# Performance work log

Hardware: AMD Instinct MI355X
Metric: run time of the kernel (lower is better)

The kernel has to match this reference:

```python
import jax, jax.numpy as jnp
import numpy as np

N, E, G, DIN, DH = 50000, 800000, 256, 128, 128
BN_EPS = 1e-5


def _gin_layer(h, src, dst, W1, b1, gamma, beta, W2, b2):
    # GINConv (eps=0): agg_i = sum_{(j->i) in edges} h_j ; z = agg + h
    agg = jnp.zeros_like(h).at[dst].add(h[src])
    z = agg + h
    z = z @ W1 + b1
    # BatchNorm1d (training mode: batch stats over nodes, biased var)
    mean = z.mean(axis=0)
    var = z.var(axis=0)
    z = gamma * (z - mean) * jax.lax.rsqrt(var + BN_EPS) + beta
    z = jax.nn.relu(z)
    z = z @ W2 + b2
    return jax.nn.relu(z)


def setup_inputs() -> dict:
    key = jax.random.key(0)
    ks = jax.random.split(key, 12)
    x = jax.random.normal(ks[0], (N, DIN), dtype=jnp.float32)
    edge_index = jax.random.randint(ks[1], (2, E), 0, N, dtype=jnp.int32)
    batch = jnp.sort(jax.random.randint(ks[2], (N,), 0, G, dtype=jnp.int32))
    s = 0.05
    W1 = jax.random.normal(ks[3], (7, DIN, DH), dtype=jnp.float32) * s
    b1 = jnp.zeros((7, DH), dtype=jnp.float32)
    gamma = jnp.ones((7, DH), dtype=jnp.float32)
    beta = jnp.zeros((7, DH), dtype=jnp.float32)
    W2 = jax.random.normal(ks[4], (7, DH, DH), dtype=jnp.float32) * s
    b2 = jnp.zeros((7, DH), dtype=jnp.float32)
    Wl1 = jax.random.normal(ks[5], (14 * DH, 14 * DH), dtype=jnp.float32) * s
    bl1 = jnp.zeros((14 * DH,), dtype=jnp.float32)
    Wl2 = jax.random.normal(ks[6], (14 * DH, 1), dtype=jnp.float32) * s
    bl2 = jnp.zeros((1,), dtype=jnp.float32)
    return {"x": x, "edge_index": edge_index, "batch": batch,
            "W1": W1, "b1": b1, "gamma": gamma, "beta": beta,
            "W2": W2, "b2": b2, "Wl1": Wl1, "bl1": bl1,
            "Wl2": Wl2, "bl2": bl2}


def reference(x, edge_index, batch, W1, b1, gamma, beta, W2, b2, Wl1, bl1, Wl2, bl2):
    src, dst = edge_index[0], edge_index[1]
    hs = []
    h = x
    for i in range(7):
        h = _gin_layer(h, src, dst, W1[i], b1[i], gamma[i], beta[i], W2[i], b2[i])
        hs.append(h)
    adds = [jax.ops.segment_sum(hi, batch, num_segments=G) for hi in hs]
    maxs = [jax.ops.segment_max(hi, batch, num_segments=G) for hi in hs]
    h = jnp.concatenate(adds + maxs, axis=1)  # [G, 14*DH]
    h = jax.nn.relu(h @ Wl1 + bl1)
    h = h @ Wl2 + bl2
    return (jax.nn.sigmoid(h), h)
```

## Files before the change

### kernel.cpp

```cpp
#include <hip/hip_runtime.h>
#include <cstdint>
#include <cstddef>

#define NN 50000
#define NE 800000
#define NG 256
#define NLAY 7
#define NBLK1 1563
#define NBUCK 16
#define CAP 18432

typedef float f32x4 __attribute__((ext_vector_type(4)));
typedef __bf16 bf16x8 __attribute__((ext_vector_type(8)));
typedef _Float16 h16x8 __attribute__((ext_vector_type(8)));

__device__ __forceinline__ float4 ld4(const float* p) { return *(const float4*)p; }
__device__ __forceinline__ void addh8(float4& x, float4& y, h16x8 v) {
  x.x += (float)v[0]; x.y += (float)v[1]; x.z += (float)v[2]; x.w += (float)v[3];
  y.x += (float)v[4]; y.y += (float)v[5]; y.z += (float)v[6]; y.w += (float)v[7];
}

__global__ void k_init(const float* __restrict__ x, const float* __restrict__ W1,
                       const float* __restrict__ W2, int* __restrict__ counts,
                       int* __restrict__ gcur, float* __restrict__ pooled,
                       _Float16* __restrict__ hb,
                       __bf16* __restrict__ w1f, __bf16* __restrict__ w2f,
                       float* __restrict__ psums) {
  int i = blockIdx.x * 256 + threadIdx.x;
  if (i < NN) counts[i] = 0;
  if (i < 49) gcur[i] = i * CAP;
  if (i < NLAY * NBUCK * 256) psums[i] = 0.f;
  if (i < NG * 1792) pooled[i] = 0.f;
  if (i < NN * 128) hb[i] = (_Float16)x[i];
  if (i < NLAY * 32768) {
    int l = i >> 15, pos = i & 32767;
    int j = pos & 7, ln = (pos >> 3) & 63, slot = (pos >> 9) & 15, kc = pos >> 13;
    int hl = slot & 1, ctp = (slot >> 1) & 3, hfp = slot >> 3;
    int n = hfp * 64 + ctp * 16 + (ln & 15);
    int k = kc * 32 + ((ln >> 4) << 3) + j;
    float a = W1[l * 16384 + k * 128 + n];
    float b = W2[l * 16384 + k * 128 + n];
    __bf16 ah = (__bf16)a, bh = (__bf16)b;
    w1f[i] = hl ? (__bf16)(a - (float)ah) : ah;
    w2f[i] = hl ? (__bf16)(b - (float)bh) : bh;
  }
}

__global__ void k_hist(const int* __restrict__ edge, int* __restrict__ counts) {
  int e = blockIdx.x * 256 + threadIdx.x;
  if (e < NE) atomicAdd(&counts[edge[NE + e]], 1);
}

__global__ void k_part(const int* __restrict__ counts, int* __restrict__ bsum) {
  __shared__ int sm[256];
  int b = blockIdx.x, t = threadIdx.x;
  int i = b * 256 + t;
  sm[t] = (i < NN) ? counts[i] : 0;
  __syncthreads();
  for (int s = 128; s > 0; s >>= 1) {
    if (t < s) sm[t] += sm[t + s];
    __syncthreads();
  }
  if (t == 0) bsum[b] = sm[0];
}

__global__ void k_bscan(const int* __restrict__ bsum, int* __restrict__ boff,
                        int* __restrict__ row_ptr) {
  __shared__ int sm[256];
  int t = threadIdx.x;
  int v = (t < 196) ? bsum[t] : 0;
  sm[t] = v;
  __syncthreads();
  int val = v;
  for (int off = 1; off < 256; off <<= 1) {
    int o = (t >= off) ? sm[t - off] : 0;
    __syncthreads();
    val += o;
    sm[t] = val;
    __syncthreads();
  }
  if (t < 196) boff[t] = val - v;
  if (t == 255) row_ptr[NN] = val;
}

__global__ void k_rowptr(const int* __restrict__ counts, const int* __restrict__ boff,
                         int* __restrict__ row_ptr) {
  __shared__ int sm[256];
  int b = blockIdx.x, t = threadIdx.x;
  int i = b * 256 + t;
  int c = (i < NN) ? counts[i] : 0;
  sm[t] = c;
  __syncthreads();
  int val = c;
  for (int off = 1; off < 256; off <<= 1) {
    int o = (t >= off) ? sm[t - off] : 0;
    __syncthreads();
    val += o;
    sm[t] = val;
    __syncthreads();
  }
  if (i < NN) row_ptr[i] = val - c + boff[b];
}

__global__ __launch_bounds__(256) void k_binA(const int* __restrict__ edge,
                                              int* __restrict__ gcur,
                                              unsigned int* __restrict__ bins) {
  __shared__ int lh[49], lbase[49], lt[49];
  const int tid = threadIdx.x;
  const int e0 = blockIdx.x * 3125, e1 = e0 + 3125;
  if (tid < 49) { lh[tid] = 0; lt[tid] = 0; }
  __syncthreads();
  for (int e = e0 + tid; e < e1; e += 256)
    atomicAdd(&lh[edge[NE + e] >> 10], 1);
  __syncthreads();
  if (tid < 49) lbase[tid] = atomicAdd(&gcur[tid], lh[tid]);
  __syncthreads();
  for (int e = e0 + tid; e < e1; e += 256) {
    int dst = edge[NE + e], src = edge[e];
    int r = dst >> 10;
    int t = atomicAdd(&lt[r], 1);
    bins[lbase[r] + t] = ((unsigned)dst << 16) | (unsigned)src;
  }
}

__global__ __launch_bounds__(512) void k_binB(const int* __restrict__ row_ptr,
                                              const int* __restrict__ gcur,
                                              const unsigned int* __restrict__ bins,
                                              unsigned short* __restrict__ csr16) {
  __shared__ int lcur[1024];
  __shared__ unsigned short lcsr[24576];
  const int blk = blockIdx.x, tid = threadIdx.x;
  const int base = blk << 10;
  const int nn = (base + 1024 <= NN) ? 1024 : (NN - base);
  const int seg0 = row_ptr[base];
  const int seg1 = row_ptr[(base + 1024 <= NN) ? (base + 1024) : NN];
  for (int i = tid; i < nn; i += 512) lcur[i] = row_ptr[base + i] - seg0;
  __syncthreads();
  const int tot = gcur[blk] - blk * CAP;
  for (int t = tid; t < tot; t += 512) {
    unsigned int p = bins[blk * CAP + t];
    int dst = (int)(p >> 16), src = (int)(p & 0xffffu);
    int pos = atomicAdd(&lcur[dst - base], 1);
    lcsr[pos] = (unsigned short)src;
  }
  __syncthreads();
  for (int i = tid; i < seg1 - seg0; i += 512) csr16[seg0 + i] = lcsr[i];
}

__device__ __forceinline__ void split8(const float4 v0, const float4 v1,
                                       bf16x8& hi, bf16x8& lo) {
  float f[8] = {v0.x, v0.y, v0.z, v0.w, v1.x, v1.y, v1.z, v1.w};
  #pragma unroll
  for (int j = 0; j < 8; ++j) {
    __bf16 h = (__bf16)f[j];
    hi[j] = h;
    lo[j] = (__bf16)(f[j] - (float)h);
  }
}

__device__ __forceinline__ void mfma_phase32(
    int tid, const __bf16* __restrict__ wf, float (*zs)[132], f32x4 acc[2])
{
  const int wv = tid >> 6;
  const int stripe = wv >> 2, half = (wv >> 1) & 1, cpair = wv & 1;
  const int lane = tid & 63, q = lane >> 4, m = lane & 15;
  #pragma unroll
  for (int kc = 0; kc < 4; ++kc) {
    const int k0 = kc * 32 + q * 8;
    float4 v0 = *(const float4*)&zs[stripe * 16 + m][k0];
    float4 v1 = *(const float4*)&zs[stripe * 16 + m][k0 + 4];
    bf16x8 ah, al;
    split8(v0, v1, ah, al);
    #pragma unroll
    for (int j = 0; j < 2; ++j) {
      const int ct = cpair * 2 + j;
      const int sbase = (half * 4 + ct) * 2;
      const __bf16* bp = wf + (((size_t)(kc * 16 + sbase) * 64 + lane) << 3);
      bf16x8 bh = *(const bf16x8*)bp;
      bf16x8 bl = *(const bf16x8*)(bp + 512);
      acc[j] = __builtin_amdgcn_mfma_f32_16x16x32_bf16(ah, bh, acc[j], 0, 0, 0);
      acc[j] = __builtin_amdgcn_mfma_f32_16x16x32_bf16(ah, bl, acc[j], 0, 0, 0);
      acc[j] = __builtin_amdgcn_mfma_f32_16x16x32_bf16(al, bh, acc[j], 0, 0, 0);
    }
  }
  __syncthreads();
}

__global__ __launch_bounds__(512, 8) void k_fused1(
    const _Float16* __restrict__ hb, const int* __restrict__ row_ptr,
    const unsigned short* __restrict__ csr_src, const __bf16* __restrict__ wf,
    const float* __restrict__ bias, _Float16* __restrict__ zb,
    float* __restrict__ ps)
{
  __shared__ float zs[32][132];
  const int tid = threadIdx.x;
  const int m0 = blockIdx.x * 32;

  {
    const int lr = tid >> 4;
    const int sub = tid & 15;
    const int r = m0 + lr;
    const int c0 = sub << 3;
    float4 a0 = make_float4(0.f, 0.f, 0.f, 0.f), a1 = a0;
    if (r < NN) {
      addh8(a0, a1, *(const h16x8*)(hb + ((size_t)r << 7) + c0));
      int e = row_ptr[r], e1 = row_ptr[r + 1];
      for (; e + 7 < e1; e += 8) {
        const h16x8 v0 = *(const h16x8*)(hb + ((size_t)csr_src[e + 0] << 7) + c0);
        const h16x8 v1 = *(const h16x8*)(hb + ((size_t)csr_src[e + 1] << 7) + c0);
        const h16x8 v2 = *(const h16x8*)(hb + ((size_t)csr_src[e + 2] << 7) + c0);
        const h16x8 v3 = *(const h16x8*)(hb + ((size_t)csr_src[e + 3] << 7) + c0);
        const h16x8 v4 = *(const h16x8*)(hb + ((size_t)csr_src[e + 4] << 7) + c0);
        const h16x8 v5 = *(const h16x8*)(hb + ((size_t)csr_src[e + 5] << 7) + c0);
        const h16x8 v6 = *(const h16x8*)(hb + ((size_t)csr_src[e + 6] << 7) + c0);
        const h16x8 v7 = *(const h16x8*)(hb + ((size_t)csr_src[e + 7] << 7) + c0);
        h16x8 t0 = v0 + v1, t1 = v2 + v3, t2 = v4 + v5, t3 = v6 + v7;
        h16x8 u0 = t0 + t1, u1 = t2 + t3;
        addh8(a0, a1, u0 + u1);
      }
      if (e + 3 < e1) {
        const h16x8 v0 = *(const h16x8*)(hb + ((size_t)csr_src[e + 0] << 7) + c0);
        const h16x8 v1 = *(const h16x8*)(hb + ((size_t)csr_src[e + 1] << 7) + c0);
        const h16x8 v2 = *(const h16x8*)(hb + ((size_t)csr_src[e + 2] << 7) + c0);
        const h16x8 v3 = *(const h16x8*)(hb + ((size_t)csr_src[e + 3] << 7) + c0);
        h16x8 t0 = v0 + v1, t1 = v2 + v3;
        addh8(a0, a1, t0 + t1);
        e += 4;
      }
      if (e + 1 < e1) {
        const h16x8 v0 = *(const h16x8*)(hb + ((size_t)csr_src[e + 0] << 7) + c0);
        const h16x8 v1 = *(const h16x8*)(hb + ((size_t)csr_src[e + 1] << 7) + c0);
        addh8(a0, a1, v0 + v1);
        e += 2;
      }
      if (e < e1)
        addh8(a0, a1, *(const h16x8*)(hb + ((size_t)csr_src[e] << 7) + c0));
    }
    *(float4*)&zs[lr][c0 + 0] = a0;
    *(float4*)&zs[lr][c0 + 4] = a1;
  }
  __syncthreads();

  const int wv = tid >> 6;
  const int stripe = wv >> 2, half = (wv >> 1) & 1, cpair = wv & 1;
  const int lane = tid & 63, q = lane >> 4, m = lane & 15;
  f32x4 acc[2] = {};
  mfma_phase32(tid, wf, zs, acc);

  float* red_s = (float*)zs;
  float* red_q = red_s + 1152;
  const int sl = stripe * 4 + q;
  #pragma unroll
  for (int j = 0; j < 2; ++j) {
    const int ct = cpair * 2 + j;
    const int col = half * 64 + ct * 16 + m;
    const float bb = bias[col];
    float s = 0.f, qq = 0.f;
    #pragma unroll
    for (int i = 0; i < 4; ++i) {
      int r = m0 + stripe * 16 + q * 4 + i;
      if (r < NN) {
        float o = acc[j][i] + bb;
        zb[((size_t)r << 7) + col] = (_Float16)o;
        s += o; qq += o * o;
      }
    }
    red_s[col * 9 + sl] = s;
    red_q[col * 9 + sl] = qq;
  }
  __syncthreads();
  if (tid < 128) {
    float s = 0.f, qq = 0.f;
    #pragma unroll
    for (int k = 0; k < 8; ++k) {
      s += red_s[tid * 9 + k];
      qq += red_q[tid * 9 + k];
    }
    float* pb = ps + (blockIdx.x & (NBUCK - 1)) * 256;
    atomicAdd(&pb[tid], s);
    atomicAdd(&pb[128 + tid], qq);
  }
}

__global__ __launch_bounds__(512) void k_fused2(
    const _Float16* __restrict__ zb, const float* __restrict__ ps,
    const float* __restrict__ gamma, const float* __restrict__ beta,
    const __bf16* __restrict__ wf, const float* __restrict__ bias,
    _Float16* __restrict__ hb, const int* __restrict__ batch,
    float* __restrict__ pooled, int layer)
{
  __shared__ float zs[32][132];
  __shared__ float sab[256];
  const int tid = threadIdx.x;
  const int m0 = blockIdx.x * 32;

  if (tid < 128) {
    float s = 0.f, q = 0.f;
    #pragma unroll
    for (int b = 0; b < NBUCK; ++b) {
      s += ps[b * 256 + tid];
      q += ps[b * 256 + 128 + tid];
    }
    float mean = s * (1.f / NN);
    float var = q * (1.f / NN) - mean * mean;
    float rstd = rsqrtf(var + 1e-5f);
    float a = gamma[tid] * rstd;
    sab[tid] = a;
    sab[128 + tid] = beta[tid] - mean * a;
  }
  __syncthreads();

  {
    const int lr = tid >> 4;
    const int sub = tid & 15;
    const int r = m0 + lr;
    const int c0 = sub << 3;
    h16x8 u0 = {};
    if (r < NN) u0 = *(const h16x8*)(zb + ((size_t)r << 7) + c0);
    float4 v0 = make_float4((float)u0[0], (float)u0[1], (float)u0[2], (float)u0[3]);
    float4 v1 = make_float4((float)u0[4], (float)u0[5], (float)u0[6], (float)u0[7]);
    float4 s0 = *(float4*)&sab[c0], s1 = *(float4*)&sab[c0 + 4];
    float4 o0 = *(float4*)&sab[128 + c0], o1 = *(float4*)&sab[128 + c0 + 4];
    float4 y0, y1;
    y0.x = fmaxf(fmaf(s0.x, v0.x, o0.x), 0.f); y0.y = fmaxf(fmaf(s0.y, v0.y, o0.y), 0.f);
    y0.z = fmaxf(fmaf(s0.z, v0.z, o0.z), 0.f); y0.w = fmaxf(fmaf(s0.w, v0.w, o0.w), 0.f);
    y1.x = fmaxf(fmaf(s1.x, v1.x, o1.x), 0.f); y1.y = fmaxf(fmaf(s1.y, v1.y, o1.y), 0.f);
    y1.z = fmaxf(fmaf(s1.z, v1.z, o1.z), 0.f); y1.w = fmaxf(fmaf(s1.w, v1.w, o1.w), 0.f);
    *(float4*)&zs[lr][c0 + 0] = y0;
    *(float4*)&zs[lr][c0 + 4] = y1;
  }
  __syncthreads();

  const int wv = tid >> 6;
  const int stripe = wv >> 2, half = (wv >> 1) & 1, cpair = wv & 1;
  const int lane = tid & 63, q = lane >> 4, m = lane & 15;
  f32x4 acc[2] = {};
  mfma_phase32(tid, wf, zs, acc);

  int bg[4];
  #pragma unroll
  for (int i = 0; i < 4; ++i) {
    int r = m0 + stripe * 16 + q * 4 + i;
    bg[i] = (r < NN) ? batch[r] : -1;
  }
  #pragma unroll
  for (int j = 0; j < 2; ++j) {
    const int ct = cpair * 2 + j;
    const int col = half * 64 + ct * 16 + m;
    const float bb = bias[col];
    #pragma unroll
    for (int i = 0; i < 4; ++i) {
      int r = m0 + stripe * 16 + q * 4 + i;
      float v = fmaxf(acc[j][i] + bb, 0.f);
      acc[j][i] = v;
      if (r < NN) hb[((size_t)r << 7) + col] = (_Float16)v;
    }
  }

  int gstart = batch[m0];
  int gend = batch[(m0 + 31 < NN) ? (m0 + 31) : (NN - 1)];
  float* red_s = (float*)zs;
  float* red_m = red_s + 1152;
  const int sl = stripe * 4 + q;
  for (int g = gstart; g <= gend; ++g) {
    __syncthreads();
    #pragma unroll
    for (int j = 0; j < 2; ++j) {
      const int ct = cpair * 2 + j;
      const int col = half * 64 + ct * 16 + m;
      float s = 0.f, mx = 0.f;
      #pragma unroll
      for (int i = 0; i < 4; ++i) {
        if (bg[i] == g) { s += acc[j][i]; mx = fmaxf(mx, acc[j][i]); }
      }
      red_s[col * 9 + sl] = s;
      red_m[col * 9 + sl] = mx;
    }
    __syncthreads();
    if (tid < 128) {
      float s = 0.f, mx = 0.f;
      #pragma unroll
      for (int k = 0; k < 8; ++k) {
        s += red_s[tid * 9 + k];
        mx = fmaxf(mx, red_m[tid * 9 + k]);
      }
      if (s != 0.f) atomicAdd(&pooled[g * 1792 + layer * 128 + tid], s);
      if (mx != 0.f)
        atomicMax((int*)&pooled[g * 1792 + 896 + layer * 128 + tid], __float_as_int(mx));
    }
  }
}

__global__ __launch_bounds__(256) void k_wl1prep(
    const float* __restrict__ Wl1, __bf16* __restrict__ wh, __bf16* __restrict__ wl) {
  __shared__ float tile[32][33];
  const int k0 = blockIdx.x * 32, n0 = blockIdx.y * 32;
  const int lr = threadIdx.x >> 5, lc = threadIdx.x & 31;
  #pragma unroll
  for (int it = 0; it < 4; ++it) {
    int rr = lr + it * 8;
    tile[rr][lc] = Wl1[(size_t)(k0 + rr) * 1792 + n0 + lc];
  }
  __syncthreads();
  #pragma unroll
  for (int it = 0; it < 4; ++it) {
    int rr = lr + it * 8;
    float v = tile[lc][rr];
    __bf16 h = (__bf16)v;
    wh[(size_t)(n0 + rr) * 1792 + k0 + lc] = h;
    wl[(size_t)(n0 + rr) * 1792 + k0 + lc] = (__bf16)(v - (float)h);
  }
}

__global__ __launch_bounds__(256) void k_mlp1a(
    const float* __restrict__ P, const __bf16* __restrict__ wh,
    const __bf16* __restrict__ wl, float* __restrict__ part)
{
  const int tid = threadIdx.x;
  const int n0 = blockIdx.x * 64;
  const int m0 = blockIdx.y * 64;
  const int kc = blockIdx.z;
  const int kbase = kc * 448;
  const int w = tid >> 6, lane = tid & 63, q = lane >> 4, m = lane & 15;
  const int row = m0 + w * 16 + m;
  f32x4 acc[4] = {};
  const float* rp = P + (size_t)row * 1792;
  #pragma unroll 2
  for (int ks = 0; ks < 14; ++ks) {
    const int k0 = kbase + ks * 32 + q * 8;
    float4 v0 = ld4(rp + k0), v1 = ld4(rp + k0 + 4);
    bf16x8 ah, al;
    split8(v0, v1, ah, al);
    #pragma unroll
    for (int ct = 0; ct < 4; ++ct) {
      const int n = n0 + ct * 16 + m;
      bf16x8 bh = *(const bf16x8*)(wh + (size_t)n * 1792 + k0);
      bf16x8 bl = *(const bf16x8*)(wl + (size_t)n * 1792 + k0);
      acc[ct] = __builtin_amdgcn_mfma_f32_16x16x32_bf16(ah, bh, acc[ct], 0, 0, 0);
      acc[ct] = __builtin_amdgcn_mfma_f32_16x16x32_bf16(ah, bl, acc[ct], 0, 0, 0);
      acc[ct] = __builtin_amdgcn_mfma_f32_16x16x32_bf16(al, bh, acc[ct], 0, 0, 0);
    }
  }
  float* pp = part + (size_t)kc * 458752;
  #pragma unroll
  for (int ct = 0; ct < 4; ++ct) {
    const int n = n0 + ct * 16 + m;
    #pragma unroll
    for (int i = 0; i < 4; ++i) {
      int r = m0 + w * 16 + q * 4 + i;
      pp[(size_t)r * 1792 + n] = acc[ct][i];
    }
  }
}

__global__ void k_mlp2(const float* __restrict__ part, const float* __restrict__ bl1,
                       const float* __restrict__ Wl2, const float* __restrict__ bl2,
                       float* __restrict__ out) {
  __shared__ float red[256];
  int g = blockIdx.x, t = threadIdx.x;
  float p = 0.f;
  for (int k = t; k < 1792; k += 256) {
    size_t idx = (size_t)g * 1792 + k;
    float s = bl1[k];
    #pragma unroll
    for (int kc = 0; kc < 4; ++kc) s += part[(size_t)kc * 458752 + idx];
    p += fmaxf(s, 0.f) * Wl2[k];
  }
  red[t] = p;
  __syncthreads();
  for (int s = 128; s > 0; s >>= 1) {
    if (t < s) red[t] += red[t + s];
    __syncthreads();
  }
  if (t == 0) {
    float l = red[0] + bl2[0];
    out[g] = 1.f / (1.f + expf(-l));
    out[NG + g] = l;
  }
}

extern "C" void kernel_launch(void* const* d_in, const int* in_sizes, int n_in,
                              void* d_out, int out_size, void* d_ws, size_t ws_size,
                              hipStream_t stream) {
  const float* x     = (const float*)d_in[0];
  const int*   edge  = (const int*)d_in[1];
  const int*   batch = (const int*)d_in[2];
  const float* W1    = (const float*)d_in[3];
  const float* b1    = (const float*)d_in[4];
  const float* gamma = (const float*)d_in[5];
  const float* beta  = (const float*)d_in[6];
  const float* W2    = (const float*)d_in[7];
  const float* b2    = (const float*)d_in[8];
  const float* Wl1   = (const float*)d_in[9];
  const float* bl1   = (const float*)d_in[10];
  const float* Wl2   = (const float*)d_in[11];
  const float* bl2   = (const float*)d_in[12];
  float* out = (float*)d_out;

  int* wsi = (int*)d_ws;
  int* row_ptr = wsi;
  int* counts  = wsi + 50048;
  int* bsum    = wsi + 100096;
  int* boff    = wsi + 100352;
  int* gcur    = wsi + 100608;
  unsigned short* csr16 = (unsigned short*)(wsi + 100864);
  float* wsf   = (float*)(wsi + 950912);
  _Float16* zb     = (_Float16*)wsf;
  _Float16* hb     = (_Float16*)(wsf + 6400000);
  float*    part   = wsf + 9600000;
  float*    psums  = wsf + 12800000;
  float*    pooled = wsf + 13000448;
  __bf16*   w1f    = (__bf16*)(wsf + 13459200);
  __bf16*   w2f    = (__bf16*)(wsf + 13573888);
  unsigned int* bins = (unsigned int*)wsf;
  __bf16*   wl1h   = (__bf16*)wsf;
  __bf16*   wl1l   = (__bf16*)(wsf + 1605632);

  k_init<<<25000, 256, 0, stream>>>(x, W1, W2, counts, gcur, pooled, hb, w1f, w2f,
                                    psums);
  k_hist<<<3125, 256, 0, stream>>>(edge, counts);
  k_part<<<196, 256, 0, stream>>>(counts, bsum);
  k_bscan<<<1, 256, 0, stream>>>(bsum, boff, row_ptr);
  k_rowptr<<<196, 256, 0, stream>>>(counts, boff, row_ptr);
  k_binA<<<256, 256, 0, stream>>>(edge, gcur, bins);
  k_binB<<<49, 512, 0, stream>>>(row_ptr, gcur, bins, csr16);

  for (int i = 0; i < NLAY; ++i) {
    k_fused1<<<NBLK1, 512, 0, stream>>>(hb, row_ptr, csr16, w1f + i * 32768,
                                        b1 + i * 128, zb, psums + i * NBUCK * 256);
    k_fused2<<<NBLK1, 512, 0, stream>>>(zb, psums + i * NBUCK * 256, gamma + i * 128,
                                        beta + i * 128, w2f + i * 32768,
                                        b2 + i * 128, hb, batch, pooled, i);
  }
  k_wl1prep<<<dim3(56, 56), 256, 0, stream>>>(Wl1, wl1h, wl1l);
  k_mlp1a<<<dim3(28, 4, 4), 256, 0, stream>>>(pooled, wl1h, wl1l, part);
  k_mlp2<<<256, 256, 0, stream>>>(part, bl1, Wl2, bl2, out);
}
```

Before: 616.5 us.

## Build CSR row pointers inside binB, dropping global histogram and scan kernels

Removes the global degree histogram, block-sum, scan and row-pointer kernels. Each binB block now builds a shared-memory histogram of its 1024 destination nodes from the bucketed edges, does a local prefix scan, and computes its global offset by summing the preceding bucket counts from gcur. This cuts four kernel launches and a pass of global atomics over all edges, in exchange for an extra read of the bins and a serial loop over up to 48 bucket counts per block.

```diff
diff --git a/kernel.cpp b/kernel.cpp
--- a/kernel.cpp
+++ b/kernel.cpp
@@ -21,13 +21,12 @@
 }
 
 __global__ void k_init(const float* __restrict__ x, const float* __restrict__ W1,
-                       const float* __restrict__ W2, int* __restrict__ counts,
+                       const float* __restrict__ W2,
                        int* __restrict__ gcur, float* __restrict__ pooled,
                        _Float16* __restrict__ hb,
                        __bf16* __restrict__ w1f, __bf16* __restrict__ w2f,
                        float* __restrict__ psums) {
   int i = blockIdx.x * 256 + threadIdx.x;
-  if (i < NN) counts[i] = 0;
   if (i < 49) gcur[i] = i * CAP;
   if (i < NLAY * NBUCK * 256) psums[i] = 0.f;
   if (i < NG * 1792) pooled[i] = 0.f;
@@ -46,62 +45,6 @@
   }
 }
 
-__global__ void k_hist(const int* __restrict__ edge, int* __restrict__ counts) {
-  int e = blockIdx.x * 256 + threadIdx.x;
-  if (e < NE) atomicAdd(&counts[edge[NE + e]], 1);
-}
-
-__global__ void k_part(const int* __restrict__ counts, int* __restrict__ bsum) {
-  __shared__ int sm[256];
-  int b = blockIdx.x, t = threadIdx.x;
-  int i = b * 256 + t;
-  sm[t] = (i < NN) ? counts[i] : 0;
-  __syncthreads();
-  for (int s = 128; s > 0; s >>= 1) {
-    if (t < s) sm[t] += sm[t + s];
-    __syncthreads();
-  }
-  if (t == 0) bsum[b] = sm[0];
-}
-
-__global__ void k_bscan(const int* __restrict__ bsum, int* __restrict__ boff,
-                        int* __restrict__ row_ptr) {
-  __shared__ int sm[256];
-  int t = threadIdx.x;
-  int v = (t < 196) ? bsum[t] : 0;
-  sm[t] = v;
-  __syncthreads();
-  int val = v;
-  for (int off = 1; off < 256; off <<= 1) {
-    int o = (t >= off) ? sm[t - off] : 0;
-    __syncthreads();
-    val += o;
-    sm[t] = val;
-    __syncthreads();
-  }
-  if (t < 196) boff[t] = val - v;
-  if (t == 255) row_ptr[NN] = val;
-}
-
-__global__ void k_rowptr(const int* __restrict__ counts, const int* __restrict__ boff,
-                         int* __restrict__ row_ptr) {
-  __shared__ int sm[256];
-  int b = blockIdx.x, t = threadIdx.x;
-  int i = b * 256 + t;
-  int c = (i < NN) ? counts[i] : 0;
-  sm[t] = c;
-  __syncthreads();
-  int val = c;
-  for (int off = 1; off < 256; off <<= 1) {
-    int o = (t >= off) ? sm[t - off] : 0;
-    __syncthreads();
-    val += o;
-    sm[t] = val;
-    __syncthreads();
-  }
-  if (i < NN) row_ptr[i] = val - c + boff[b];
-}
-
 __global__ __launch_bounds__(256) void k_binA(const int* __restrict__ edge,
                                               int* __restrict__ gcur,
                                               unsigned int* __restrict__ bins) {
@@ -123,20 +66,44 @@
   }
 }
 
-__global__ __launch_bounds__(512) void k_binB(const int* __restrict__ row_ptr,
-                                              const int* __restrict__ gcur,
+__global__ __launch_bounds__(512) void k_binB(const int* __restrict__ gcur,
                                               const unsigned int* __restrict__ bins,
-                                              unsigned short* __restrict__ csr16) {
+                                              unsigned short* __restrict__ csr16,
+                                              int* __restrict__ row_ptr) {
+  __shared__ int lhist[1024];
   __shared__ int lcur[1024];
+  __shared__ int sm[512];
   __shared__ unsigned short lcsr[24576];
   const int blk = blockIdx.x, tid = threadIdx.x;
   const int base = blk << 10;
-  const int nn = (base + 1024 <= NN) ? 1024 : (NN - base);
-  const int seg0 = row_ptr[base];
-  const int seg1 = row_ptr[(base + 1024 <= NN) ? (base + 1024) : NN];
-  for (int i = tid; i < nn; i += 512) lcur[i] = row_ptr[base + i] - seg0;
-  __syncthreads();
   const int tot = gcur[blk] - blk * CAP;
+  int seg0 = 0;
+  for (int k = 0; k < blk; ++k) seg0 += gcur[k] - k * CAP;
+  for (int i = tid; i < 1024; i += 512) lhist[i] = 0;
+  __syncthreads();
+  for (int t = tid; t < tot; t += 512)
+    atomicAdd(&lhist[(int)(bins[blk * CAP + t] >> 16) - base], 1);
+  __syncthreads();
+  int a = lhist[2 * tid], b = lhist[2 * tid + 1];
+  int pair = a + b;
+  sm[tid] = pair;
+  __syncthreads();
+  int val = pair;
+  for (int off = 1; off < 512; off <<= 1) {
+    int o = (tid >= off) ? sm[tid - off] : 0;
+    __syncthreads();
+    val += o;
+    sm[tid] = val;
+    __syncthreads();
+  }
+  int e0 = val - pair;
+  int e1 = e0 + a;
+  lcur[2 * tid] = e0;
+  lcur[2 * tid + 1] = e1;
+  if (base + 2 * tid < NN)     row_ptr[base + 2 * tid] = seg0 + e0;
+  if (base + 2 * tid + 1 < NN) row_ptr[base + 2 * tid + 1] = seg0 + e1;
+  if (blk == 48 && tid == 0)   row_ptr[NN] = seg0 + tot;
+  __syncthreads();
   for (int t = tid; t < tot; t += 512) {
     unsigned int p = bins[blk * CAP + t];
     int dst = (int)(p >> 16), src = (int)(p & 0xffffu);
@@ -144,7 +111,7 @@
     lcsr[pos] = (unsigned short)src;
   }
   __syncthreads();
-  for (int i = tid; i < seg1 - seg0; i += 512) csr16[seg0 + i] = lcsr[i];
+  for (int i = tid; i < tot; i += 512) csr16[seg0 + i] = lcsr[i];
 }
 
 __device__ __forceinline__ void split8(const float4 v0, const float4 v1,
@@ -499,9 +466,6 @@
 
   int* wsi = (int*)d_ws;
   int* row_ptr = wsi;
-  int* counts  = wsi + 50048;
-  int* bsum    = wsi + 100096;
-  int* boff    = wsi + 100352;
   int* gcur    = wsi + 100608;
   unsigned short* csr16 = (unsigned short*)(wsi + 100864);
   float* wsf   = (float*)(wsi + 950912);
@@ -516,14 +480,9 @@
   __bf16*   wl1h   = (__bf16*)wsf;
   __bf16*   wl1l   = (__bf16*)(wsf + 1605632);
 
-  k_init<<<25000, 256, 0, stream>>>(x, W1, W2, counts, gcur, pooled, hb, w1f, w2f,
-                                    psums);
-  k_hist<<<3125, 256, 0, stream>>>(edge, counts);
-  k_part<<<196, 256, 0, stream>>>(counts, bsum);
-  k_bscan<<<1, 256, 0, stream>>>(bsum, boff, row_ptr);
-  k_rowptr<<<196, 256, 0, stream>>>(counts, boff, row_ptr);
+  k_init<<<25000, 256, 0, stream>>>(x, W1, W2, gcur, pooled, hb, w1f, w2f, psums);
   k_binA<<<256, 256, 0, stream>>>(edge, gcur, bins);
-  k_binB<<<49, 512, 0, stream>>>(row_ptr, gcur, bins, csr16);
+  k_binB<<<49, 512, 0, stream>>>(gcur, bins, csr16, row_ptr);
 
   for (int i = 0; i < NLAY; ++i) {
     k_fused1<<<NBLK1, 512, 0, stream>>>(hb, row_ptr, csr16, w1f + i * 32768,
```

New measurement: 579.7 us. 1.06x faster.
